# Kernel tuning notes

Hardware: AMD Instinct MI355X
Metric: run time of the kernel (lower is better)

Reference implementation:

```python
import jax, jax.numpy as jnp
import numpy as np

NUM_USERS = 100000
NUM_ITEMS = 50000
HIDDEN = 64
NUM_LAYERS = 3
NUM_EDGES = 1200000
N = NUM_USERS + NUM_ITEMS


def setup_inputs() -> dict:
    key = jax.random.key(0)
    k_e, k_u, k_i, k_w, k_b = jax.random.split(key, 5)
    edge_index = jax.random.randint(k_e, (2, NUM_EDGES), 0, N, dtype=jnp.int32)
    users_emb = jax.random.normal(k_u, (NUM_USERS, HIDDEN), dtype=jnp.float32) * 0.01
    items_emb = jax.random.normal(k_i, (NUM_ITEMS, HIDDEN), dtype=jnp.float32) * 0.01
    # GCNConv linear weights (glorot-ish) and zero biases, stacked over layers
    scale = 1.0 / np.sqrt(HIDDEN)
    Ws = jax.random.uniform(k_w, (NUM_LAYERS, HIDDEN, HIDDEN), dtype=jnp.float32,
                            minval=-scale, maxval=scale)
    bs = jnp.zeros((NUM_LAYERS, HIDDEN), dtype=jnp.float32)
    return {"edge_index": edge_index, "users_emb": users_emb,
            "items_emb": items_emb, "Ws": Ws, "bs": bs}


def reference(edge_index, users_emb, items_emb, Ws, bs):
    # GraphSAGEModel.forward: concat user/item embeddings, run num_layers GCNConv
    # (PyG defaults: add self-loops, symmetric D^-1/2 A D^-1/2 normalization, bias).
    x = jnp.concatenate([users_emb, items_emb], axis=0)  # [N, H]

    self_loops = jnp.arange(N, dtype=edge_index.dtype)
    src = jnp.concatenate([edge_index[0], self_loops])  # [E+N]
    dst = jnp.concatenate([edge_index[1], self_loops])

    ones = jnp.ones(src.shape[0], dtype=x.dtype)
    deg = jax.ops.segment_sum(ones, dst, num_segments=N)  # in-degree incl self loop
    dinv = jnp.where(deg > 0, jax.lax.rsqrt(deg), 0.0)
    norm = dinv[src] * dinv[dst]  # [E+N], graph-constant across layers

    for l in range(NUM_LAYERS):
        h = x @ Ws[l]                       # linear transform [N, H]
        msg = h[src] * norm[:, None]        # gather + scale
        x = jax.ops.segment_sum(msg, dst, num_segments=N) + bs[l]
    return (x[:NUM_USERS], users_emb, x[NUM_USERS:], items_emb)
```

## Files before the change

kernel.cpp:

```cpp
#include <hip/hip_runtime.h>
#include <hip/hip_fp16.h>
#include <type_traits>

#define NU 100000
#define NI 50000
#define NN 150000
#define HH 64
#define NE 1200000

#define SCAN_CHUNK 1024
#define NBLK ((NN + SCAN_CHUNK - 1) / SCAN_CHUNK)

__global__ __launch_bounds__(256) void k_rank(const int4* __restrict__ dst4,
                                              int* __restrict__ counts,
                                              int4* __restrict__ rank4,
                                              __half* __restrict__ xs_pad) {
    if (blockIdx.x == 0 && threadIdx.x < 8)
        ((int4*)xs_pad)[threadIdx.x] = make_int4(0, 0, 0, 0);
    int t = blockIdx.x * blockDim.x + threadIdx.x;
    if (t >= NE / 8) return;
    int4 d0 = dst4[2 * t], d1 = dst4[2 * t + 1];
    int4 r0, r1;
    r0.x = atomicAdd(&counts[d0.x], 1);
    r0.y = atomicAdd(&counts[d0.y], 1);
    r0.z = atomicAdd(&counts[d0.z], 1);
    r0.w = atomicAdd(&counts[d0.w], 1);
    r1.x = atomicAdd(&counts[d1.x], 1);
    r1.y = atomicAdd(&counts[d1.y], 1);
    r1.z = atomicAdd(&counts[d1.z], 1);
    r1.w = atomicAdd(&counts[d1.w], 1);
    rank4[2 * t]     = r0;
    rank4[2 * t + 1] = r1;
}

__global__ __launch_bounds__(256) void k_scan(const int* __restrict__ counts,
                                              float* __restrict__ dinv,
                                              int* __restrict__ row_ptr,
                                              unsigned int* __restrict__ state) {
    __shared__ int sd[256];
    __shared__ int s_prefix;
    int t = threadIdx.x;
    int b = blockIdx.x;
    int base = b * SCAN_CHUNK + t * 4;
    int c[4];
    if (base + 3 < NN) {
        int4 v = *(const int4*)(counts + base);
        c[0] = v.x; c[1] = v.y; c[2] = v.z; c[3] = v.w;
    } else {
#pragma unroll
        for (int i = 0; i < 4; ++i) c[i] = (base + i < NN) ? counts[base + i] : 0;
    }
#pragma unroll
    for (int i = 0; i < 4; ++i)
        if (base + i < NN) dinv[base + i] = rsqrtf((float)(c[i] + 1));

    int tt = c[0] + c[1] + c[2] + c[3];
    sd[t] = tt; __syncthreads();
    for (int off = 1; off < 256; off <<= 1) {
        int x = (t >= off) ? sd[t - off] : 0;
        __syncthreads();
        sd[t] += x;
        __syncthreads();
    }

    if (t == 0) {
        unsigned int agg = (unsigned int)sd[255];
        if (b == 0) {
            __hip_atomic_store(&state[0], (2u << 30) | agg, __ATOMIC_RELEASE,
                               __HIP_MEMORY_SCOPE_AGENT);
            s_prefix = 0;
        } else {
            __hip_atomic_store(&state[b], (1u << 30) | agg, __ATOMIC_RELEASE,
                               __HIP_MEMORY_SCOPE_AGENT);
            unsigned int prefix = 0;
            int p = b - 1;
            while (true) {
                unsigned int s = __hip_atomic_load(&state[p], __ATOMIC_ACQUIRE,
                                                   __HIP_MEMORY_SCOPE_AGENT);
                unsigned int fl = s >> 30;
                if (fl == 0u) continue;
                prefix += s & 0x3FFFFFFFu;
                if (fl == 2u) break;
                --p;
            }
            __hip_atomic_store(&state[b], (2u << 30) | (prefix + agg),
                               __ATOMIC_RELEASE, __HIP_MEMORY_SCOPE_AGENT);
            s_prefix = (int)prefix;
        }
    }
    __syncthreads();

    int off0 = s_prefix + (sd[t] - tt);
    int run = 0;
#pragma unroll
    for (int i = 0; i < 4; ++i) {
        if (base + i < NN) row_ptr[base + i] = off0 + run;
        run += c[i];
    }
    if (b == NBLK - 1 && t == 0) row_ptr[NN] = NE;
}

#define CONCAT_BLOCKS (NN * (HH / 4) / 256)
#define FILL_BLOCKS   ((NE / 8 + 255) / 256)

__global__ __launch_bounds__(256) void k_concat_fill(
    const float4* __restrict__ users, const float4* __restrict__ items,
    const float* __restrict__ dinv, __half2* __restrict__ xs, float4* __restrict__ out,
    const int4* __restrict__ src4, const int4* __restrict__ dst4,
    const int4* __restrict__ rank4, const int* __restrict__ row_ptr,
    int* __restrict__ col) {
    if (blockIdx.x < CONCAT_BLOCKS) {
        int i = blockIdx.x * 256 + threadIdx.x;
        const int UB = NU * (HH / 4);
        float4 v;
        if (i < UB) {
            v = users[i];
            out[UB + i] = v;
        } else {
            int j = i - UB;
            v = items[j];
            out[2 * UB + NI * (HH / 4) + j] = v;
        }
        float dv = dinv[i >> 4];
        xs[2 * i]     = __halves2half2(__float2half_rn(v.x * dv), __float2half_rn(v.y * dv));
        xs[2 * i + 1] = __halves2half2(__float2half_rn(v.z * dv), __float2half_rn(v.w * dv));
    } else {
        int t = (blockIdx.x - CONCAT_BLOCKS) * 256 + threadIdx.x;
        if (t >= NE / 8) return;
        int4 s0 = src4[2 * t],  s1 = src4[2 * t + 1];
        int4 d0 = dst4[2 * t],  d1 = dst4[2 * t + 1];
        int4 r0 = rank4[2 * t], r1 = rank4[2 * t + 1];
        int p0 = row_ptr[d0.x], p1 = row_ptr[d0.y], p2 = row_ptr[d0.z], p3 = row_ptr[d0.w];
        int p4 = row_ptr[d1.x], p5 = row_ptr[d1.y], p6 = row_ptr[d1.z], p7 = row_ptr[d1.w];
        col[p0 + r0.x] = s0.x;
        col[p1 + r0.y] = s0.y;
        col[p2 + r0.z] = s0.z;
        col[p3 + r0.w] = s0.w;
        col[p4 + r1.x] = s1.x;
        col[p5 + r1.y] = s1.y;
        col[p6 + r1.z] = s1.z;
        col[p7 + r1.w] = s1.w;
    }
}

__global__ __launch_bounds__(256) void k_aggregate(const __half* __restrict__ x,
                                                   __half* __restrict__ y,
                                                   const float* __restrict__ dinv,
                                                   const int* __restrict__ row_ptr,
                                                   const int* __restrict__ col) {
    int lane = threadIdx.x & 63;
    int wave = blockIdx.x * 4 + (threadIdx.x >> 6);
    int na = wave * 2;
    if (na >= NN) return;
    int nb = na + 1;
    int q  = lane >> 4;
    int f4 = (lane & 15) << 2;

    float a0 = 0.f, a1 = 0.f, a2 = 0.f, a3 = 0.f;
    float b0 = 0.f, b1 = 0.f, b2 = 0.f, b3 = 0.f;

#define GATHER(r, c0, c1, c2, c3)                                          \
    {                                                                      \
        uint2 raw = *(const uint2*)(x + (size_t)(r) * HH + f4);            \
        float2 f0 = __half22float2(*(__half2*)&raw.x);                     \
        float2 f1 = __half22float2(*(__half2*)&raw.y);                     \
        c0 += f0.x; c1 += f0.y; c2 += f1.x; c3 += f1.y;                    \
    }

    int ea = row_ptr[na], enda = row_ptr[na + 1];
    int eb = enda,        endb = row_ptr[nb + 1];

    {
        int ia = ea + q - 1;
        int ib = eb + q - 1;
        int rA = (q == 0) ? na : ((ia < enda) ? col[ia] : NN);
        int rB = (q == 0) ? nb : ((ib < endb) ? col[ib] : NN);
        GATHER(rA, a0, a1, a2, a3);
        GATHER(rB, b0, b1, b2, b3);
        ea += 3; eb += 3;
    }
    while (ea < enda || eb < endb) {
        int iA1 = ea + q,     iA2 = ea + 4 + q;
        int iB1 = eb + q,     iB2 = eb + 4 + q;
        int rA1 = (iA1 < enda) ? col[iA1] : NN;
        int rA2 = (iA2 < enda) ? col[iA2] : NN;
        int rB1 = (iB1 < endb) ? col[iB1] : NN;
        int rB2 = (iB2 < endb) ? col[iB2] : NN;
        GATHER(rA1, a0, a1, a2, a3);
        GATHER(rA2, a0, a1, a2, a3);
        GATHER(rB1, b0, b1, b2, b3);
        GATHER(rB2, b0, b1, b2, b3);
        ea += 8; eb += 8;
    }
#undef GATHER

    a0 += __shfl_xor(a0, 16); a1 += __shfl_xor(a1, 16);
    a2 += __shfl_xor(a2, 16); a3 += __shfl_xor(a3, 16);
    b0 += __shfl_xor(b0, 16); b1 += __shfl_xor(b1, 16);
    b2 += __shfl_xor(b2, 16); b3 += __shfl_xor(b3, 16);
    a0 += __shfl_xor(a0, 32); a1 += __shfl_xor(a1, 32);
    a2 += __shfl_xor(a2, 32); a3 += __shfl_xor(a3, 32);
    b0 += __shfl_xor(b0, 32); b1 += __shfl_xor(b1, 32);
    b2 += __shfl_xor(b2, 32); b3 += __shfl_xor(b3, 32);

    if (lane < 32) {
        int   n  = (q == 0) ? na : nb;
        float dv = dinv[n];
        float s0 = (q == 0) ? a0 : b0;
        float s1 = (q == 0) ? a1 : b1;
        float s2 = (q == 0) ? a2 : b2;
        float s3 = (q == 0) ? a3 : b3;
        __half2 h0 = __halves2half2(__float2half_rn(dv * s0), __float2half_rn(dv * s1));
        __half2 h1 = __halves2half2(__float2half_rn(dv * s2), __float2half_rn(dv * s3));
        uint2 packed;
        packed.x = *(unsigned int*)&h0;
        packed.y = *(unsigned int*)&h1;
        *(uint2*)(y + (size_t)n * HH + f4) = packed;
    }
}

#define GR 128
#define XSS 65
template <typename OutT>
__global__ __launch_bounds__(256) void k_gemm(const __half* __restrict__ y,
                                              const float* __restrict__ W,
                                              const float* __restrict__ b,
                                              const float* __restrict__ dinv,
                                              OutT* __restrict__ out_lo,
                                              OutT* __restrict__ out_hi,
                                              int split) {
    __shared__ float xs[GR * XSS];
    __shared__ float ws[HH * HH];
    int t = threadIdx.x;
    int rowBase = blockIdx.x * GR;

    {
        const float4* W4 = (const float4*)W;
        float4* ws4 = (float4*)ws;
#pragma unroll
        for (int i = 0; i < 4; ++i) ws4[i * 256 + t] = W4[i * 256 + t];
    }
#pragma unroll
    for (int it = 0; it < 4; ++it) {
        int g = it * 256 + t;
        int r = g >> 3;
        int c0 = (g & 7) * 8;
        int row = rowBase + r;
        if (row < NN) {
            int4 raw = *(const int4*)(y + (size_t)row * HH + c0);
            __half2 h0 = *(__half2*)&raw.x, h1 = *(__half2*)&raw.y;
            __half2 h2 = *(__half2*)&raw.z, h3 = *(__half2*)&raw.w;
            float2 f0 = __half22float2(h0), f1 = __half22float2(h1);
            float2 f2 = __half22float2(h2), f3 = __half22float2(h3);
            float* dp = xs + r * XSS + c0;
            dp[0] = f0.x; dp[1] = f0.y; dp[2] = f1.x; dp[3] = f1.y;
            dp[4] = f2.x; dp[5] = f2.y; dp[6] = f3.x; dp[7] = f3.y;
        }
    }
    __syncthreads();

    int tx = t & 7;
    int ty = t >> 3;
    int j0 = tx * 8;
    int r0 = ty * 4;

    float acc[4][8];
#pragma unroll
    for (int i = 0; i < 4; ++i)
#pragma unroll
        for (int j = 0; j < 8; ++j) acc[i][j] = 0.f;

    for (int k = 0; k < HH; ++k) {
        float4 w0 = *(const float4*)(ws + k * HH + j0);
        float4 w1 = *(const float4*)(ws + k * HH + j0 + 4);
        float wv[8] = {w0.x, w0.y, w0.z, w0.w, w1.x, w1.y, w1.z, w1.w};
#pragma unroll
        for (int i = 0; i < 4; ++i) {
            float xv = xs[(r0 + i) * XSS + k];
#pragma unroll
            for (int j = 0; j < 8; ++j) acc[i][j] += xv * wv[j];
        }
    }

    float bj[8];
#pragma unroll
    for (int j = 0; j < 8; ++j) bj[j] = b[j0 + j];

#pragma unroll
    for (int i = 0; i < 4; ++i) {
        int r = rowBase + r0 + i;
        if (r >= NN) continue;
        if constexpr (std::is_same_v<OutT, float>) {
            float4 o0 = make_float4(acc[i][0] + bj[0], acc[i][1] + bj[1],
                                    acc[i][2] + bj[2], acc[i][3] + bj[3]);
            float4 o1 = make_float4(acc[i][4] + bj[4], acc[i][5] + bj[5],
                                    acc[i][6] + bj[6], acc[i][7] + bj[7]);
            float* d = (r < split) ? ((float*)out_lo + (size_t)r * HH)
                                   : ((float*)out_hi + (size_t)(r - split) * HH);
            *(float4*)(d + j0) = o0;
            *(float4*)(d + j0 + 4) = o1;
        } else {
            float dv = dinv[r];
            __half2 h[4];
#pragma unroll
            for (int j = 0; j < 4; ++j)
                h[j] = __halves2half2(
                    __float2half_rn((acc[i][2 * j]     + bj[2 * j])     * dv),
                    __float2half_rn((acc[i][2 * j + 1] + bj[2 * j + 1]) * dv));
            __half* d = (__half*)out_lo + (size_t)r * HH + j0;
            *(int4*)d = *(int4*)h;
        }
    }
}

extern "C" void kernel_launch(void* const* d_in, const int* in_sizes, int n_in,
                              void* d_out, int out_size, void* d_ws, size_t ws_size,
                              hipStream_t stream) {
    const int*   edge  = (const int*)d_in[0];
    const int*   src   = edge;
    const int*   dst   = edge + NE;
    const float* users = (const float*)d_in[1];
    const float* items = (const float*)d_in[2];
    const float* Ws    = (const float*)d_in[3];
    const float* bs    = (const float*)d_in[4];
    float*       out   = (float*)d_out;

    char* w = (char*)d_ws;
    __half* Xs0     = (__half*)w; w += (size_t)(NN + 1) * HH * 2;
    __half* Xs1     = (__half*)w; w += (size_t)(NN + 1) * HH * 2;
    float*  dinv    = (float*)w;  w += (size_t)NN * 4;
    unsigned int* state = (unsigned int*)w; w += 256 * 4;
    int*    counts  = (int*)w;    w += (size_t)NN * 4;
    int*    row_ptr = (int*)w;    w += (size_t)(NN + 1) * 4;
    w += 12;
    int*    col     = (int*)w;    w += (size_t)NE * 4;
    int*    rank    = (int*)w;    w += (size_t)NE * 4;
    (void)ws_size; (void)in_sizes; (void)n_in; (void)out_size;

    hipMemsetAsync(state, 0, (size_t)(256 + NN) * sizeof(int), stream);

    k_rank<<<(NE / 8 + 255) / 256, 256, 0, stream>>>(
        (const int4*)dst, counts, (int4*)rank, Xs0 + (size_t)NN * HH);
    k_scan<<<NBLK, 256, 0, stream>>>(counts, dinv, row_ptr, state);
    k_concat_fill<<<CONCAT_BLOCKS + FILL_BLOCKS, 256, 0, stream>>>(
        (const float4*)users, (const float4*)items, dinv, (__half2*)Xs0, (float4*)out,
        (const int4*)src, (const int4*)dst, (const int4*)rank, row_ptr, col);

    const int AGG_BLOCKS  = NN / 8;
    const int GEMM_BLOCKS = (NN + GR - 1) / GR;

    k_aggregate<<<AGG_BLOCKS, 256, 0, stream>>>(Xs0, Xs1, dinv, row_ptr, col);
    k_gemm<__half><<<GEMM_BLOCKS, 256, 0, stream>>>(
        Xs1, Ws + 0 * HH * HH, bs + 0 * HH, dinv, Xs0, Xs0, NN);
    k_aggregate<<<AGG_BLOCKS, 256, 0, stream>>>(Xs0, Xs1, dinv, row_ptr, col);
    k_gemm<__half><<<GEMM_BLOCKS, 256, 0, stream>>>(
        Xs1, Ws + 1 * HH * HH, bs + 1 * HH, dinv, Xs0, Xs0, NN);
    k_aggregate<<<AGG_BLOCKS, 256, 0, stream>>>(Xs0, Xs1, dinv, row_ptr, col);
    k_gemm<float><<<GEMM_BLOCKS, 256, 0, stream>>>(
        Xs1, Ws + 2 * HH * HH, bs + 2 * HH, dinv,
        out , out + (size_t)2 * NU * HH , NU);
}
```

Baseline: 433.0 us.

## Collapse three linear layers into one fused weight and final GEMM

Uses linearity of the GCN stack: all three propagations are applied first, then a single GEMM with the premultiplied W0·W1·W2 runs, with bias terms carried through scalar propagations (u1, u2) of the all-ones vector. Two of the three per-layer dense GEMM launches are removed, and the precomputed weight product is folded into an extra block of the first aggregate launch. Intermediate features stay in fp16 across three unscaled-by-W propagations, so rounding error may behave differently. A sleep is also added in the scan's spin loop.

After: 414.5 us. -4.3%, faster.

```diff
diff --git a/kernel.cpp b/kernel.cpp
--- a/kernel.cpp
+++ b/kernel.cpp
@@ -1,6 +1,5 @@
 #include <hip/hip_runtime.h>
 #include <hip/hip_fp16.h>
-#include <type_traits>
 
 #define NU 100000
 #define NI 50000
@@ -10,13 +9,18 @@
 
 #define SCAN_CHUNK 1024
 #define NBLK ((NN + SCAN_CHUNK - 1) / SCAN_CHUNK)
+#define AGG_BLOCKS (NN / 8)
+#define UBLK ((NN + 255) / 256)
 
 __global__ __launch_bounds__(256) void k_rank(const int4* __restrict__ dst4,
                                               int* __restrict__ counts,
                                               int4* __restrict__ rank4,
-                                              __half* __restrict__ xs_pad) {
-    if (blockIdx.x == 0 && threadIdx.x < 8)
-        ((int4*)xs_pad)[threadIdx.x] = make_int4(0, 0, 0, 0);
+                                              __half* __restrict__ pad0,
+                                              __half* __restrict__ pad1) {
+    if (blockIdx.x == 0 && threadIdx.x < 16) {
+        if (threadIdx.x < 8) ((int4*)pad0)[threadIdx.x] = make_int4(0, 0, 0, 0);
+        else                 ((int4*)pad1)[threadIdx.x - 8] = make_int4(0, 0, 0, 0);
+    }
     int t = blockIdx.x * blockDim.x + threadIdx.x;
     if (t >= NE / 8) return;
     int4 d0 = dst4[2 * t], d1 = dst4[2 * t + 1];
@@ -35,6 +39,7 @@
 
 __global__ __launch_bounds__(256) void k_scan(const int* __restrict__ counts,
                                               float* __restrict__ dinv,
+                                              float* __restrict__ dinv2,
                                               int* __restrict__ row_ptr,
                                               unsigned int* __restrict__ state) {
     __shared__ int sd[256];
@@ -52,7 +57,10 @@
     }
 #pragma unroll
     for (int i = 0; i < 4; ++i)
-        if (base + i < NN) dinv[base + i] = rsqrtf((float)(c[i] + 1));
+        if (base + i < NN) {
+            dinv[base + i]  = rsqrtf((float)(c[i] + 1));
+            dinv2[base + i] = 1.0f / (float)(c[i] + 1);
+        }
 
     int tt = c[0] + c[1] + c[2] + c[3];
     sd[t] = tt; __syncthreads();
@@ -78,7 +86,7 @@
                 unsigned int s = __hip_atomic_load(&state[p], __ATOMIC_ACQUIRE,
                                                    __HIP_MEMORY_SCOPE_AGENT);
                 unsigned int fl = s >> 30;
-                if (fl == 0u) continue;
+                if (fl == 0u) { __builtin_amdgcn_s_sleep(1); continue; }
                 prefix += s & 0x3FFFFFFFu;
                 if (fl == 2u) break;
                 --p;
@@ -143,13 +151,77 @@
     }
 }
 
-__global__ __launch_bounds__(256) void k_aggregate(const __half* __restrict__ x,
-                                                   __half* __restrict__ y,
-                                                   const float* __restrict__ dinv,
-                                                   const int* __restrict__ row_ptr,
-                                                   const int* __restrict__ col) {
+template <int MODE>
+__global__ __launch_bounds__(256) void k_aggregate(
+    const __half* __restrict__ x, __half* __restrict__ y,
+    const float* __restrict__ scale,
+    const int* __restrict__ row_ptr, const int* __restrict__ col,
+    const float* __restrict__ dinv, const float* __restrict__ pin,
+    float* __restrict__ uout, float* __restrict__ pout,
+    const float* __restrict__ Wfull, const float* __restrict__ bfull,
+    float* __restrict__ What, float* __restrict__ cvec) {
+    int bid = blockIdx.x;
+    if (MODE != 0) {
+        const int EXTRA = (MODE == 1) ? (UBLK + 1) : UBLK;
+        if (bid < EXTRA) {
+            if (MODE == 1 && bid == UBLK) {
+                __shared__ float W12[HH * HH];
+                int t = threadIdx.x;
+                int r = t >> 2, j0 = (t & 3) * 16;
+                const float* W0 = Wfull;
+                const float* W1 = Wfull + HH * HH;
+                const float* W2 = Wfull + 2 * HH * HH;
+                float acc[16];
+#pragma unroll
+                for (int j = 0; j < 16; ++j) acc[j] = 0.f;
+                for (int k = 0; k < HH; ++k) {
+                    float a = W1[r * HH + k];
+                    const float* bp = W2 + k * HH + j0;
+#pragma unroll
+                    for (int j = 0; j < 16; ++j) acc[j] += a * bp[j];
+                }
+#pragma unroll
+                for (int j = 0; j < 16; ++j) W12[r * HH + j0 + j] = acc[j];
+                if (t < HH) {
+                    float s = 0.f;
+                    for (int k = 0; k < HH; ++k) s += bfull[HH + k] * W2[k * HH + t];
+                    cvec[HH + t] = s;
+                }
+                __syncthreads();
+#pragma unroll
+                for (int j = 0; j < 16; ++j) acc[j] = 0.f;
+                for (int k = 0; k < HH; ++k) {
+                    float a = W0[r * HH + k];
+                    const float* bp = W12 + k * HH + j0;
+#pragma unroll
+                    for (int j = 0; j < 16; ++j) acc[j] += a * bp[j];
+                }
+#pragma unroll
+                for (int j = 0; j < 16; ++j) What[r * HH + j0 + j] = acc[j];
+                if (t < HH) {
+                    float s = 0.f;
+                    for (int k = 0; k < HH; ++k) s += bfull[k] * W12[k * HH + t];
+                    cvec[t] = s;
+                }
+                return;
+            }
+            int n = bid * 256 + threadIdx.x;
+            if (n < NN) {
+                float dv = dinv[n];
+                float acc = pin[n];
+                int e1 = row_ptr[n + 1];
+                for (int e = row_ptr[n]; e < e1; ++e) acc += pin[col[e]];
+                float u = dv * acc;
+                uout[n] = u;
+                if (MODE == 1) pout[n] = dv * u;
+            }
+            return;
+        }
+        bid -= EXTRA;
+    }
+
     int lane = threadIdx.x & 63;
-    int wave = blockIdx.x * 4 + (threadIdx.x >> 6);
+    int wave = bid * 4 + (threadIdx.x >> 6);
     int na = wave * 2;
     if (na >= NN) return;
     int nb = na + 1;
@@ -205,7 +277,7 @@
 
     if (lane < 32) {
         int   n  = (q == 0) ? na : nb;
-        float dv = dinv[n];
+        float dv = scale[n];
         float s0 = (q == 0) ? a0 : b0;
         float s1 = (q == 0) ? a1 : b1;
         float s2 = (q == 0) ? a2 : b2;
@@ -221,14 +293,11 @@
 
 #define GR 128
 #define XSS 65
-template <typename OutT>
-__global__ __launch_bounds__(256) void k_gemm(const __half* __restrict__ y,
-                                              const float* __restrict__ W,
-                                              const float* __restrict__ b,
-                                              const float* __restrict__ dinv,
-                                              OutT* __restrict__ out_lo,
-                                              OutT* __restrict__ out_hi,
-                                              int split) {
+__global__ __launch_bounds__(256) void k_gemm_final(
+    const __half* __restrict__ y, const float* __restrict__ W,
+    const float* __restrict__ b2, const float* __restrict__ cvec,
+    const float* __restrict__ u1, const float* __restrict__ u2,
+    float* __restrict__ out_lo, float* __restrict__ out_hi) {
     __shared__ float xs[GR * XSS];
     __shared__ float ws[HH * HH];
     int t = threadIdx.x;
@@ -282,34 +351,30 @@
         }
     }
 
-    float bj[8];
-#pragma unroll
-    for (int j = 0; j < 8; ++j) bj[j] = b[j0 + j];
+    float c0j[8], c1j[8], b2j[8];
+#pragma unroll
+    for (int j = 0; j < 8; ++j) {
+        c0j[j] = cvec[j0 + j];
+        c1j[j] = cvec[HH + j0 + j];
+        b2j[j] = b2[j0 + j];
+    }
 
 #pragma unroll
     for (int i = 0; i < 4; ++i) {
         int r = rowBase + r0 + i;
         if (r >= NN) continue;
-        if constexpr (std::is_same_v<OutT, float>) {
-            float4 o0 = make_float4(acc[i][0] + bj[0], acc[i][1] + bj[1],
-                                    acc[i][2] + bj[2], acc[i][3] + bj[3]);
-            float4 o1 = make_float4(acc[i][4] + bj[4], acc[i][5] + bj[5],
-                                    acc[i][6] + bj[6], acc[i][7] + bj[7]);
-            float* d = (r < split) ? ((float*)out_lo + (size_t)r * HH)
-                                   : ((float*)out_hi + (size_t)(r - split) * HH);
-            *(float4*)(d + j0) = o0;
-            *(float4*)(d + j0 + 4) = o1;
-        } else {
-            float dv = dinv[r];
-            __half2 h[4];
-#pragma unroll
-            for (int j = 0; j < 4; ++j)
-                h[j] = __halves2half2(
-                    __float2half_rn((acc[i][2 * j]     + bj[2 * j])     * dv),
-                    __float2half_rn((acc[i][2 * j + 1] + bj[2 * j + 1]) * dv));
-            __half* d = (__half*)out_lo + (size_t)r * HH + j0;
-            *(int4*)d = *(int4*)h;
-        }
+        float u2r = u2[r], u1r = u1[r];
+        float base[8];
+#pragma unroll
+        for (int j = 0; j < 8; ++j) base[j] = u2r * c0j[j] + u1r * c1j[j] + b2j[j];
+        float4 o0 = make_float4(acc[i][0] + base[0], acc[i][1] + base[1],
+                                acc[i][2] + base[2], acc[i][3] + base[3]);
+        float4 o1 = make_float4(acc[i][4] + base[4], acc[i][5] + base[5],
+                                acc[i][6] + base[6], acc[i][7] + base[7]);
+        float* d = (r < NU) ? (out_lo + (size_t)r * HH)
+                            : (out_hi + (size_t)(r - NU) * HH);
+        *(float4*)(d + j0) = o0;
+        *(float4*)(d + j0 + 4) = o1;
     }
 }
 
@@ -329,6 +394,12 @@
     __half* Xs0     = (__half*)w; w += (size_t)(NN + 1) * HH * 2;
     __half* Xs1     = (__half*)w; w += (size_t)(NN + 1) * HH * 2;
     float*  dinv    = (float*)w;  w += (size_t)NN * 4;
+    float*  dinv2   = (float*)w;  w += (size_t)NN * 4;
+    float*  u1      = (float*)w;  w += (size_t)NN * 4;
+    float*  p1u     = (float*)w;  w += (size_t)NN * 4;
+    float*  u2      = (float*)w;  w += (size_t)NN * 4;
+    float*  What    = (float*)w;  w += (size_t)HH * HH * 4;
+    float*  cvec    = (float*)w;  w += (size_t)2 * HH * 4;
     unsigned int* state = (unsigned int*)w; w += 256 * 4;
     int*    counts  = (int*)w;    w += (size_t)NN * 4;
     int*    row_ptr = (int*)w;    w += (size_t)(NN + 1) * 4;
@@ -340,23 +411,24 @@
     hipMemsetAsync(state, 0, (size_t)(256 + NN) * sizeof(int), stream);
 
     k_rank<<<(NE / 8 + 255) / 256, 256, 0, stream>>>(
-        (const int4*)dst, counts, (int4*)rank, Xs0 + (size_t)NN * HH);
-    k_scan<<<NBLK, 256, 0, stream>>>(counts, dinv, row_ptr, state);
+        (const int4*)dst, counts, (int4*)rank,
+        Xs0 + (size_t)NN * HH, Xs1 + (size_t)NN * HH);
+    k_scan<<<NBLK, 256, 0, stream>>>(counts, dinv, dinv2, row_ptr, state);
     k_concat_fill<<<CONCAT_BLOCKS + FILL_BLOCKS, 256, 0, stream>>>(
         (const float4*)users, (const float4*)items, dinv, (__half2*)Xs0, (float4*)out,
         (const int4*)src, (const int4*)dst, (const int4*)rank, row_ptr, col);
 
-    const int AGG_BLOCKS  = NN / 8;
+    k_aggregate<1><<<UBLK + 1 + AGG_BLOCKS, 256, 0, stream>>>(
+        Xs0, Xs1, dinv2, row_ptr, col, dinv, dinv, u1, p1u, Ws, bs, What, cvec);
+    k_aggregate<2><<<UBLK + AGG_BLOCKS, 256, 0, stream>>>(
+        Xs1, Xs0, dinv2, row_ptr, col, dinv, p1u, u2, nullptr, nullptr, nullptr,
+        nullptr, nullptr);
+    k_aggregate<0><<<AGG_BLOCKS, 256, 0, stream>>>(
+        Xs0, Xs1, dinv, row_ptr, col, nullptr, nullptr, nullptr, nullptr, nullptr,
+        nullptr, nullptr, nullptr);
+
     const int GEMM_BLOCKS = (NN + GR - 1) / GR;
-
-    k_aggregate<<<AGG_BLOCKS, 256, 0, stream>>>(Xs0, Xs1, dinv, row_ptr, col);
-    k_gemm<__half><<<GEMM_BLOCKS, 256, 0, stream>>>(
-        Xs1, Ws + 0 * HH * HH, bs + 0 * HH, dinv, Xs0, Xs0, NN);
-    k_aggregate<<<AGG_BLOCKS, 256, 0, stream>>>(Xs0, Xs1, dinv, row_ptr, col);
-    k_gemm<__half><<<GEMM_BLOCKS, 256, 0, stream>>>(
-        Xs1, Ws + 1 * HH * HH, bs + 1 * HH, dinv, Xs0, Xs0, NN);
-    k_aggregate<<<AGG_BLOCKS, 256, 0, stream>>>(Xs0, Xs1, dinv, row_ptr, col);
-    k_gemm<float><<<GEMM_BLOCKS, 256, 0, stream>>>(
-        Xs1, Ws + 2 * HH * HH, bs + 2 * HH, dinv,
-        out , out + (size_t)2 * NU * HH , NU);
-}
+    k_gemm_final<<<GEMM_BLOCKS, 256, 0, stream>>>(
+        Xs1, What, bs + 2 * HH, cvec, u1, u2,
+        out , out + (size_t)2 * NU * HH );
+}
```
